# Kernel optimization log

Measured on AMD Instinct MI355X. Metric: run time of the kernel, lower is better.

## Reference

```python
import jax, jax.numpy as jnp
import numpy as np

EMBED_DIM = 512
NUM_HEADS = 8
GAMMA = 0.1


def setup_inputs() -> dict:
    key = jax.random.key(0)
    ks = jax.random.split(key, 16)
    B, T, D, Hp, Wp = 4, 16, EMBED_DIM, 24, 24
    Dq = D // 4
    s = 1.0 / np.sqrt(D)
    inp = {
        "h_opt": jax.random.normal(ks[0], (B, T, D, Hp, Wp), jnp.float32),
        "h_sar": jax.random.normal(ks[1], (B, T, D, Hp, Wp), jnp.float32),
        "Wq": jax.random.normal(ks[2], (D, D), jnp.float32) * s,
        "bq": jnp.zeros((D,), jnp.float32),
        "Wk": jax.random.normal(ks[3], (D, D), jnp.float32) * s,
        "bk": jnp.zeros((D,), jnp.float32),
        "Wv": jax.random.normal(ks[4], (D, D), jnp.float32) * s,
        "bv": jnp.zeros((D,), jnp.float32),
        "Wo": jax.random.normal(ks[5], (D, D), jnp.float32) * s,
        "bo": jnp.zeros((D,), jnp.float32),
        "Wp1": jax.random.normal(ks[6], (D, Dq), jnp.float32) * s,
        "bp1": jnp.zeros((Dq,), jnp.float32),
        "Wp2": jax.random.normal(ks[7], (Dq, 1), jnp.float32) * (1.0 / np.sqrt(Dq)),
        "bp2": jnp.zeros((1,), jnp.float32),
    }
    return inp


def reference(h_opt, h_sar, Wq, bq, Wk, bk, Wv, bv, Wo, bo, Wp1, bp1, Wp2, bp2):
    B, T, D, Hp, Wp_ = h_opt.shape
    S = Hp * Wp_
    H = NUM_HEADS
    hd = D // H

    # (B,T,D,H',W') -> (B*S, T, D): each spatial location is an independent sequence over T
    opt_seq = jnp.transpose(h_opt, (0, 3, 4, 1, 2)).reshape(B * S, T, D)
    sar_seq = jnp.transpose(h_sar, (0, 3, 4, 1, 2)).reshape(B * S, T, D)

    Q = (opt_seq @ Wq + bq).reshape(B * S, T, H, hd)
    K = (sar_seq @ Wk + bk).reshape(B * S, T, H, hd)
    V = (sar_seq @ Wv + bv).reshape(B * S, T, H, hd)

    # scores: (N, H, Tq, Tk)
    scores = jnp.einsum("nthd,nshd->nhts", Q, K) / np.sqrt(hd).astype(np.float32)

    # per-key physical violation penalty: MLP(sar) -> sigmoid in [0,1], shape (N, Tk)
    hdn = jax.nn.gelu(sar_seq @ Wp1 + bp1, approximate=False)
    p_viol = jax.nn.sigmoid((hdn @ Wp2 + bp2).squeeze(-1))  # (N, T)
    scores = scores - GAMMA * p_viol[:, None, None, :]

    attn = jax.nn.softmax(scores, axis=-1)  # dropout is identity in eval mode
    out = jnp.einsum("nhts,nshd->nthd", attn, V).reshape(B * S, T, D)
    out = out @ Wo + bo
    return jnp.transpose(out.reshape(B, Hp, Wp_, T, D), (0, 3, 4, 1, 2))
```

## Files before the change

### kernel.cpp

```cpp
#include <hip/hip_runtime.h>

#define GAMMA 0.1f

typedef unsigned short u16;
typedef u16 u16x8 __attribute__((ext_vector_type(8)));
typedef short s16x8 __attribute__((ext_vector_type(8)));
typedef float f32x4 __attribute__((ext_vector_type(4)));
typedef unsigned int ui32x4 __attribute__((ext_vector_type(4)));

__device__ __forceinline__ float b2f(u16 u) {
  return __uint_as_float(((unsigned)u) << 16);
}
__device__ __forceinline__ u16 f2bf(float f) {
  unsigned u = __float_as_uint(f);
  unsigned r = (u + 0x7FFFu + ((u >> 16) & 1u)) >> 16;
  return (u16)r;
}
__device__ __forceinline__ unsigned pk_bf16(float lo, float hi) {
  return (unsigned)f2bf(lo) | ((unsigned)f2bf(hi) << 16);
}

__device__ __forceinline__ void gl2lds16(const u16* g, u16* l) {
  __builtin_amdgcn_global_load_lds(
      (const __attribute__((address_space(1))) unsigned int*)g,
      (__attribute__((address_space(3))) unsigned int*)l, 16, 0, 0);
}

__device__ __forceinline__ int xcd_swz(int phys, int nwg) {
  return (phys & 7) * (nwg >> 3) + (phys >> 3);
}

__global__ __launch_bounds__(256) void transpose_k(
    const float* __restrict__ src, u16* __restrict__ dst, int K, int N)
{
  int idx = blockIdx.x * 256 + threadIdx.x;
  if (idx >= K * N) return;
  int nn = idx / K, kk = idx - nn * K;
  dst[idx] = f2bf(src[kk * N + nn]);
}

__global__ __launch_bounds__(256) void bias_kernel(
    const float* __restrict__ bq, const float* __restrict__ bk,
    const float* __restrict__ bv, const float* __restrict__ bp1,
    const float* __restrict__ bo,
    float* __restrict__ biasQ, float* __restrict__ biasKVP,
    float* __restrict__ biasO)
{
  int i = blockIdx.x * 256 + threadIdx.x;
  if (i < 512) {
    biasQ[i] = bq[i];
  } else if (i < 1664) {
    int j = i - 512;
    float v;
    if (j < 512) v = bk[j];
    else if (j < 1024) v = bv[j - 512];
    else v = bp1[j - 1024];
    biasKVP[j] = v;
  } else if (i < 2176) {
    biasO[i - 1664] = bo[i - 1664];
  }
}

__global__ __launch_bounds__(256) void convert_h(
    const float* __restrict__ h0, const float* __restrict__ h1,
    u16* __restrict__ d0, u16* __restrict__ d1)
{
  __shared__ __align__(16) u16 T[64 * 64];
  const int tid = threadIdx.x;
  const int kt = blockIdx.x & 7, st = blockIdx.x >> 3;
  const int bt = blockIdx.y;
  const float* src = (blockIdx.z ? h1 : h0) + (size_t)bt * (512 * 576);
  u16* dst = (blockIdx.z ? d1 : d0) + (size_t)bt * (576 * 512);

  const int s = tid & 63, kc = tid >> 6;
  const float* sp = src + (size_t)(kt * 64 + kc * 16) * 576 + st * 64 + s;
  unsigned pk[8];
#pragma unroll
  for (int i = 0; i < 8; ++i) {
    float lo = sp[(2 * i) * 576];
    float hi = sp[(2 * i + 1) * 576];
    pk[i] = pk_bf16(lo, hi);
  }
  ui32x4 v0 = {pk[0], pk[1], pk[2], pk[3]};
  ui32x4 v1 = {pk[4], pk[5], pk[6], pk[7]};
  *(ui32x4*)&T[s * 64 + (((kc * 2)     ^ (s & 7)) * 8)] = v0;
  *(ui32x4*)&T[s * 64 + (((kc * 2 + 1) ^ (s & 7)) * 8)] = v1;
  __syncthreads();
  const int r = tid >> 2, oc = (tid & 3) * 2;
  ui32x4 w0 = *(const ui32x4*)&T[r * 64 + ((oc       ^ (r & 7)) * 8)];
  ui32x4 w1 = *(const ui32x4*)&T[r * 64 + (((oc + 1) ^ (r & 7)) * 8)];
  u16* dp = dst + (size_t)(st * 64 + r) * 512 + kt * 64 + oc * 8;
  *(ui32x4*)dp = w0;
  *(ui32x4*)(dp + 8) = w1;
}

__global__ __launch_bounds__(256) void gemm_proj(
    const u16* __restrict__ hT, const u16* __restrict__ WT,
    const float* __restrict__ bias, u16* __restrict__ C, int NC)
{
  __shared__ __align__(16) u16 Al[2][64 * 64];
  __shared__ __align__(16) u16 Bl[2][128 * 64];
  const int tid = threadIdx.x;
  const int w = tid >> 6, lane = tid & 63;
  const int lhi = lane >> 4, llo = lane & 15;

  const int nwg = gridDim.x * gridDim.y;
  const int phys = blockIdx.y * gridDim.x + blockIdx.x;
  const int logical = xcd_swz(phys, nwg);
  const int bx = logical % gridDim.x;
  const int y = logical / gridDim.x;

  const int bt = y / 9, stile = y - bt * 9;
  const int s0 = stile * 64;
  const int col0 = bx * 128;

  const u16* Ab = hT + (size_t)bt * (576 * 512) + (size_t)s0 * 512;
  const u16* Bb = WT + (size_t)col0 * 512;

  const int brow = lane >> 3;
  const int bko = ((lane & 7) ^ brow) * 8;

  f32x4 acc[4][2];
#pragma unroll
  for (int mi = 0; mi < 4; ++mi)
#pragma unroll
    for (int ni = 0; ni < 2; ++ni)
#pragma unroll
      for (int e = 0; e < 4; ++e) acc[mi][ni][e] = 0.f;

#pragma unroll
  for (int i = 0; i < 2; ++i) {
    int q = w * 2 + i;
    gl2lds16(Ab + (size_t)(q * 8 + brow) * 512 + bko, &Al[0][q * 512]);
  }
#pragma unroll
  for (int i = 0; i < 4; ++i) {
    int q = w * 4 + i;
    gl2lds16(Bb + (size_t)(q * 8 + brow) * 512 + bko, &Bl[0][q * 512]);
  }

  for (int kt = 0; kt < 8; ++kt) {
    __syncthreads();
    if (kt < 7) {
      const int ktn = kt + 1;
#pragma unroll
      for (int i = 0; i < 2; ++i) {
        int q = w * 2 + i;
        gl2lds16(Ab + (size_t)(q * 8 + brow) * 512 + ktn * 64 + bko,
                 &Al[ktn & 1][q * 512]);
      }
#pragma unroll
      for (int i = 0; i < 4; ++i) {
        int q = w * 4 + i;
        gl2lds16(Bb + (size_t)(q * 8 + brow) * 512 + ktn * 64 + bko,
                 &Bl[ktn & 1][q * 512]);
      }
    }
    const u16* Alc = Al[kt & 1];
    const u16* Blc = Bl[kt & 1];
#pragma unroll
    for (int hh = 0; hh < 2; ++hh) {
      s16x8 af[4], bfr[2];
#pragma unroll
      for (int mi = 0; mi < 4; ++mi) {
        int row = mi * 16 + llo;
        af[mi] = *(const s16x8*)&Alc[row * 64 + ((((hh << 2) | lhi) ^ (row & 7)) * 8)];
      }
#pragma unroll
      for (int ni = 0; ni < 2; ++ni) {
        int n = w * 32 + ni * 16 + llo;
        bfr[ni] = *(const s16x8*)&Blc[n * 64 + ((((hh << 2) | lhi) ^ (n & 7)) * 8)];
      }
#pragma unroll
      for (int mi = 0; mi < 4; ++mi)
#pragma unroll
        for (int ni = 0; ni < 2; ++ni)
          acc[mi][ni] = __builtin_amdgcn_mfma_f32_16x16x32_bf16(
              af[mi], bfr[ni], acc[mi][ni], 0, 0, 0);
    }
  }

  const int b_ = bt >> 4, t_ = bt & 15;
  const size_t rowbase = (size_t)(b_ * 576 + s0) * 16 + t_;
  float bia0 = bias[col0 + w * 32 + llo];
  float bia1 = bias[col0 + w * 32 + 16 + llo];
#pragma unroll
  for (int mi = 0; mi < 4; ++mi) {
#pragma unroll
    for (int i = 0; i < 4; ++i) {
      const int m = mi * 16 + lhi * 4 + i;
      u16* cp = C + (rowbase + (size_t)m * 16) * NC + col0 + w * 32 + llo;
      cp[0]  = f2bf(acc[mi][0][i] + bia0);
      cp[16] = f2bf(acc[mi][1][i] + bia1);
    }
  }
}

__global__ __launch_bounds__(256) void pviol_kernel(
    const u16* __restrict__ KVP, const float* __restrict__ Wp2,
    const float* __restrict__ bp2, float* __restrict__ pv)
{
  const int tid = threadIdx.x;
  const int w = tid >> 6, lane = tid & 63;
  const int row = blockIdx.x * 4 + w;
  const int c = lane * 2;
  const u16* hp = KVP + (size_t)row * 1152 + 1024 + c;
  float x0 = b2f(hp[0]), x1 = b2f(hp[1]);
  float g0 = 0.5f * x0 * (1.f + erff(x0 * 0.70710678f));
  float g1 = 0.5f * x1 * (1.f + erff(x1 * 0.70710678f));
  float sum = g0 * Wp2[c] + g1 * Wp2[c + 1];
#pragma unroll
  for (int d = 1; d < 64; d <<= 1) sum += __shfl_xor(sum, d, 64);
  if (lane == 0) {
    float z = sum + bp2[0];
    pv[row] = 1.f / (1.f + expf(-z));
  }
}

__global__ __launch_bounds__(256) void attn_kernel(
    const u16* Q, const u16* __restrict__ KVP,
    const float* __restrict__ pviol, u16* att)
{
  __shared__ __align__(16) u16 Kl[4][16 * 72];
  __shared__ __align__(16) u16 Vl[4][16 * 72];
  __shared__ float Pl[4][16 * 17];
  const int tid = threadIdx.x;
  const int w = tid >> 6, lane = tid & 63;
  const int logical = xcd_swz(blockIdx.x, gridDim.x);
  const int wid = logical * 4 + w;
  const int n = wid >> 3, hh = wid & 7;
  const int g = lane >> 4, tq = lane & 15;

  const int r = lane >> 3, co = (lane & 7) * 8;
  const u16* Kb = KVP + (size_t)n * (16 * 1152) + hh * 64;
#pragma unroll
  for (int rr = 0; rr < 2; ++rr) {
    int row = r + rr * 8;
    *(u16x8*)&Kl[w][row * 72 + co] = *(const u16x8*)(Kb + row * 1152 + co);
    *(u16x8*)&Vl[w][row * 72 + co] = *(const u16x8*)(Kb + 512 + row * 1152 + co);
  }
  __syncthreads();

  float s[4] = {0.f, 0.f, 0.f, 0.f};
  const u16* Qr = Q + ((size_t)n * 16 + tq) * 512 + hh * 64;
  for (int kc = 0; kc < 8; ++kc) {
    u16x8 q8 = *(const u16x8*)(Qr + kc * 8);
    float qf[8];
#pragma unroll
    for (int j = 0; j < 8; ++j) qf[j] = b2f(q8[j]);
#pragma unroll
    for (int i = 0; i < 4; ++i) {
      u16x8 k8 = *(const u16x8*)&Kl[w][(g * 4 + i) * 72 + kc * 8];
#pragma unroll
      for (int j = 0; j < 8; ++j) s[i] += qf[j] * b2f(k8[j]);
    }
  }

  const float* pv = pviol + n * 16;
#pragma unroll
  for (int i = 0; i < 4; ++i) s[i] = s[i] * 0.125f - GAMMA * pv[g * 4 + i];

  float mx = fmaxf(fmaxf(s[0], s[1]), fmaxf(s[2], s[3]));
  mx = fmaxf(mx, __shfl_xor(mx, 16, 64));
  mx = fmaxf(mx, __shfl_xor(mx, 32, 64));
  float e[4], sum = 0.f;
#pragma unroll
  for (int i = 0; i < 4; ++i) { e[i] = expf(s[i] - mx); sum += e[i]; }
  sum += __shfl_xor(sum, 16, 64);
  sum += __shfl_xor(sum, 32, 64);
  float inv = 1.f / sum;
#pragma unroll
  for (int i = 0; i < 4; ++i) Pl[w][tq * 17 + g * 4 + i] = e[i] * inv;
  __syncthreads();

  float o[16];
#pragma unroll
  for (int j = 0; j < 16; ++j) o[j] = 0.f;
  for (int tk = 0; tk < 16; ++tk) {
    float p = Pl[w][tq * 17 + tk];
    u16x8 v0 = *(const u16x8*)&Vl[w][tk * 72 + g * 16];
    u16x8 v1 = *(const u16x8*)&Vl[w][tk * 72 + g * 16 + 8];
#pragma unroll
    for (int j = 0; j < 8; ++j) {
      o[j]     += p * b2f(v0[j]);
      o[8 + j] += p * b2f(v1[j]);
    }
  }
  u16* op = att + ((size_t)n * 16 + tq) * 512 + hh * 64 + g * 16;
  u16x8 r0, r1;
#pragma unroll
  for (int j = 0; j < 8; ++j) { r0[j] = f2bf(o[j]); r1[j] = f2bf(o[8 + j]); }
  *(u16x8*)op = r0;
  *(u16x8*)(op + 8) = r1;
}

__global__ __launch_bounds__(256) void gemm_out(
    const u16* __restrict__ A, const u16* __restrict__ WT,
    const float* __restrict__ bias, float* __restrict__ out)
{
  __shared__ __align__(16) char smem[49152];
  u16* Al0 = (u16*)smem;
  u16* Bl0 = (u16*)(smem + 16384);
  const int tid = threadIdx.x;
  const int w = tid >> 6, lane = tid & 63;
  const int lhi = lane >> 4, llo = lane & 15;

  const int nwg = gridDim.x * gridDim.y;
  const int phys = blockIdx.y * gridDim.x + blockIdx.x;
  const int logical = xcd_swz(phys, nwg);
  const int bx = logical % gridDim.x;
  const int y = logical / gridDim.x;

  const int bt = y / 9, stile = y - bt * 9;
  const int s0 = stile * 64;
  const int col0 = bx * 128;
  const int b_ = bt >> 4, t_ = bt & 15;

  const u16* Ab = A + ((size_t)(b_ * 576 + s0) * 16 + t_) * 512;
  const u16* Bb = WT + (size_t)col0 * 512;

  const int brow = lane >> 3;
  const int bko = ((lane & 7) ^ brow) * 8;

  f32x4 acc[4][2];
#pragma unroll
  for (int mi = 0; mi < 4; ++mi)
#pragma unroll
    for (int ni = 0; ni < 2; ++ni)
#pragma unroll
      for (int e = 0; e < 4; ++e) acc[mi][ni][e] = 0.f;

#pragma unroll
  for (int i = 0; i < 2; ++i) {
    int q = w * 2 + i;
    gl2lds16(Ab + (size_t)(q * 8 + brow) * (16 * 512) + bko, &Al0[q * 512]);
  }
#pragma unroll
  for (int i = 0; i < 4; ++i) {
    int q = w * 4 + i;
    gl2lds16(Bb + (size_t)(q * 8 + brow) * 512 + bko, &Bl0[q * 512]);
  }

  for (int kt = 0; kt < 8; ++kt) {
    __syncthreads();
    if (kt < 7) {
      const int ktn = kt + 1;
      u16* Ala = Al0 + (ktn & 1) * (64 * 64);
      u16* Bla = Bl0 + (ktn & 1) * (128 * 64);
#pragma unroll
      for (int i = 0; i < 2; ++i) {
        int q = w * 2 + i;
        gl2lds16(Ab + (size_t)(q * 8 + brow) * (16 * 512) + ktn * 64 + bko,
                 &Ala[q * 512]);
      }
#pragma unroll
      for (int i = 0; i < 4; ++i) {
        int q = w * 4 + i;
        gl2lds16(Bb + (size_t)(q * 8 + brow) * 512 + ktn * 64 + bko,
                 &Bla[q * 512]);
      }
    }
    const u16* Alc = Al0 + (kt & 1) * (64 * 64);
    const u16* Blc = Bl0 + (kt & 1) * (128 * 64);
#pragma unroll
    for (int hh = 0; hh < 2; ++hh) {
      s16x8 af[4], bfr[2];
#pragma unroll
      for (int mi = 0; mi < 4; ++mi) {
        int row = mi * 16 + llo;
        af[mi] = *(const s16x8*)&Alc[row * 64 + ((((hh << 2) | lhi) ^ (row & 7)) * 8)];
      }
#pragma unroll
      for (int ni = 0; ni < 2; ++ni) {
        int n = w * 32 + ni * 16 + llo;
        bfr[ni] = *(const s16x8*)&Blc[n * 64 + ((((hh << 2) | lhi) ^ (n & 7)) * 8)];
      }
#pragma unroll
      for (int mi = 0; mi < 4; ++mi)
#pragma unroll
        for (int ni = 0; ni < 2; ++ni)
          acc[mi][ni] = __builtin_amdgcn_mfma_f32_16x16x32_bf16(
              af[mi], bfr[ni], acc[mi][ni], 0, 0, 0);
    }
  }

  __syncthreads();
  float* Cl = (float*)smem;
  float bia0 = bias[col0 + w * 32 + llo];
  float bia1 = bias[col0 + w * 32 + 16 + llo];
#pragma unroll
  for (int mi = 0; mi < 4; ++mi)
#pragma unroll
    for (int i = 0; i < 4; ++i) {
      int m = mi * 16 + lhi * 4 + i;
      Cl[(w * 32 + llo) * 72 + m]      = acc[mi][0][i] + bia0;
      Cl[(w * 32 + 16 + llo) * 72 + m] = acc[mi][1][i] + bia1;
    }
  __syncthreads();
  const int nn = tid >> 1;
  const int mh = (tid & 1) * 32;
  const float* sp = Cl + nn * 72 + mh;
  float* dp = out + ((size_t)bt * 512 + col0 + nn) * 576 + s0 + mh;
#pragma unroll
  for (int j = 0; j < 8; ++j)
    *(float4*)(dp + j * 4) = *(const float4*)(sp + j * 4);
}

extern "C" void kernel_launch(void* const* d_in, const int* in_sizes, int n_in,
                              void* d_out, int out_size, void* d_ws, size_t ws_size,
                              hipStream_t stream)
{
  const float* h_opt = (const float*)d_in[0];
  const float* h_sar = (const float*)d_in[1];
  const float* Wq  = (const float*)d_in[2];
  const float* bq  = (const float*)d_in[3];
  const float* Wk  = (const float*)d_in[4];
  const float* bk  = (const float*)d_in[5];
  const float* Wv  = (const float*)d_in[6];
  const float* bv  = (const float*)d_in[7];
  const float* Wo  = (const float*)d_in[8];
  const float* bo  = (const float*)d_in[9];
  const float* Wp1 = (const float*)d_in[10];
  const float* bp1 = (const float*)d_in[11];
  const float* Wp2 = (const float*)d_in[12];
  const float* bp2 = (const float*)d_in[13];
  float* out = (float*)d_out;

  char* ws = (char*)d_ws;
  u16*   WqT     = (u16*)(ws + 0);
  u16*   KVPW    = (u16*)(ws + 524288);
  u16*   WoT     = (u16*)(ws + 1703936);
  float* biasQ   = (float*)(ws + 2228224);
  float* biasKVP = (float*)(ws + 2230272);
  float* biasO   = (float*)(ws + 2234880);
  float* pviol   = (float*)(ws + 2236928);
  u16*   Qbuf    = (u16*)(ws + 2384384);
  u16*   KVPbuf  = (u16*)(ws + 40133120);
  u16*   hTopt   = (u16*)(ws + 125067776);
  u16*   hTsar   = (u16*)(ws + 162816512);

  transpose_k<<<1024, 256, 0, stream>>>(Wq, WqT, 512, 512);
  transpose_k<<<1024, 256, 0, stream>>>(Wk, KVPW, 512, 512);
  transpose_k<<<1024, 256, 0, stream>>>(Wv, KVPW + 512 * 512, 512, 512);
  transpose_k<<<256, 256, 0, stream>>>(Wp1, KVPW + 1024 * 512, 512, 128);
  transpose_k<<<1024, 256, 0, stream>>>(Wo, WoT, 512, 512);
  bias_kernel<<<9, 256, 0, stream>>>(bq, bk, bv, bp1, bo, biasQ, biasKVP, biasO);
  convert_h<<<dim3(72, 64, 2), 256, 0, stream>>>(h_opt, h_sar, hTopt, hTsar);

  gemm_proj<<<dim3(4, 576), 256, 0, stream>>>(hTopt, WqT, biasQ, Qbuf, 512);
  gemm_proj<<<dim3(9, 576), 256, 0, stream>>>(hTsar, KVPW, biasKVP, KVPbuf, 1152);
  pviol_kernel<<<9216, 256, 0, stream>>>(KVPbuf, Wp2, bp2, pviol);
  attn_kernel<<<4608, 256, 0, stream>>>(Qbuf, KVPbuf, pviol, Qbuf);
  gemm_out<<<dim3(4, 576), 256, 0, stream>>>(Qbuf, WoT, biasO, out);
}
```

Before: 427.3 us.

## Merge prep kernels, fuse Q and KVP projections, fold p_viol MLP into GEMM epilogue

Seven prep launches (weight transposes, bias copies, h conversion) become one kernel that picks its role from the block index. The Q and K/V/P1 projection GEMMs are merged into a single 13-column grid. The GELU+Wp2+sigmoid violation head is computed in the epilogue of the P1 column tile, which removes the separate pviol kernel and the bf16 write and reread of the P1 hidden activations. This cuts launch overhead and memory traffic, and keeps the hidden activations in fp32 instead of rounding them to bf16. The cost is extra branching, extra shared memory and shuffle reductions in the GEMM kernel.

```diff
diff --git a/kernel.cpp b/kernel.cpp
--- a/kernel.cpp
+++ b/kernel.cpp
@@ -30,92 +30,130 @@
   return (phys & 7) * (nwg >> 3) + (phys >> 3);
 }
 
-__global__ __launch_bounds__(256) void transpose_k(
-    const float* __restrict__ src, u16* __restrict__ dst, int K, int N)
+#define PREP_NCONV 9216
+#define PREP_T0 9216
+#define PREP_T1 10240
+#define PREP_T2 11264
+#define PREP_T3 12288
+#define PREP_T4 12544
+#define PREP_T5 13568
+#define PREP_NB 13577
+
+__device__ __forceinline__ void tr_block(
+    const float* __restrict__ src, u16* __restrict__ dst, int N, int blk, int tid)
 {
-  int idx = blockIdx.x * 256 + threadIdx.x;
-  if (idx >= K * N) return;
-  int nn = idx / K, kk = idx - nn * K;
+  int idx = blk * 256 + tid;
+  int nn = idx >> 9, kk = idx & 511;
   dst[idx] = f2bf(src[kk * N + nn]);
 }
 
-__global__ __launch_bounds__(256) void bias_kernel(
+__global__ __launch_bounds__(256) void prep_all(
+    const float* __restrict__ h0, const float* __restrict__ h1,
+    u16* __restrict__ d0, u16* __restrict__ d1,
+    const float* __restrict__ Wq, const float* __restrict__ Wk,
+    const float* __restrict__ Wv, const float* __restrict__ Wp1,
+    const float* __restrict__ Wo,
     const float* __restrict__ bq, const float* __restrict__ bk,
     const float* __restrict__ bv, const float* __restrict__ bp1,
     const float* __restrict__ bo,
+    u16* __restrict__ WqT, u16* __restrict__ KVPW, u16* __restrict__ WoT,
     float* __restrict__ biasQ, float* __restrict__ biasKVP,
     float* __restrict__ biasO)
 {
-  int i = blockIdx.x * 256 + threadIdx.x;
-  if (i < 512) {
-    biasQ[i] = bq[i];
-  } else if (i < 1664) {
-    int j = i - 512;
-    float v;
-    if (j < 512) v = bk[j];
-    else if (j < 1024) v = bv[j - 512];
-    else v = bp1[j - 1024];
-    biasKVP[j] = v;
-  } else if (i < 2176) {
-    biasO[i - 1664] = bo[i - 1664];
-  }
-}
-
-__global__ __launch_bounds__(256) void convert_h(
-    const float* __restrict__ h0, const float* __restrict__ h1,
-    u16* __restrict__ d0, u16* __restrict__ d1)
-{
   __shared__ __align__(16) u16 T[64 * 64];
+  const int b = blockIdx.x;
   const int tid = threadIdx.x;
-  const int kt = blockIdx.x & 7, st = blockIdx.x >> 3;
-  const int bt = blockIdx.y;
-  const float* src = (blockIdx.z ? h1 : h0) + (size_t)bt * (512 * 576);
-  u16* dst = (blockIdx.z ? d1 : d0) + (size_t)bt * (576 * 512);
-
-  const int s = tid & 63, kc = tid >> 6;
-  const float* sp = src + (size_t)(kt * 64 + kc * 16) * 576 + st * 64 + s;
-  unsigned pk[8];
-#pragma unroll
-  for (int i = 0; i < 8; ++i) {
-    float lo = sp[(2 * i) * 576];
-    float hi = sp[(2 * i + 1) * 576];
-    pk[i] = pk_bf16(lo, hi);
-  }
-  ui32x4 v0 = {pk[0], pk[1], pk[2], pk[3]};
-  ui32x4 v1 = {pk[4], pk[5], pk[6], pk[7]};
-  *(ui32x4*)&T[s * 64 + (((kc * 2)     ^ (s & 7)) * 8)] = v0;
-  *(ui32x4*)&T[s * 64 + (((kc * 2 + 1) ^ (s & 7)) * 8)] = v1;
-  __syncthreads();
-  const int r = tid >> 2, oc = (tid & 3) * 2;
-  ui32x4 w0 = *(const ui32x4*)&T[r * 64 + ((oc       ^ (r & 7)) * 8)];
-  ui32x4 w1 = *(const ui32x4*)&T[r * 64 + (((oc + 1) ^ (r & 7)) * 8)];
-  u16* dp = dst + (size_t)(st * 64 + r) * 512 + kt * 64 + oc * 8;
-  *(ui32x4*)dp = w0;
-  *(ui32x4*)(dp + 8) = w1;
-}
-
-__global__ __launch_bounds__(256) void gemm_proj(
-    const u16* __restrict__ hT, const u16* __restrict__ WT,
-    const float* __restrict__ bias, u16* __restrict__ C, int NC)
+
+  if (b < PREP_NCONV) {
+    const int z = b / 4608;
+    const int r_ = b - z * 4608;
+    const int bt = r_ / 72;
+    const int xx = r_ - bt * 72;
+    const int kt = xx & 7, st = xx >> 3;
+    const float* src = (z ? h1 : h0) + (size_t)bt * (512 * 576);
+    u16* dst = (z ? d1 : d0) + (size_t)bt * (576 * 512);
+
+    const int s = tid & 63, kc = tid >> 6;
+    const float* sp = src + (size_t)(kt * 64 + kc * 16) * 576 + st * 64 + s;
+    unsigned pk[8];
+#pragma unroll
+    for (int i = 0; i < 8; ++i) {
+      float lo = sp[(2 * i) * 576];
+      float hi = sp[(2 * i + 1) * 576];
+      pk[i] = pk_bf16(lo, hi);
+    }
+    ui32x4 v0 = {pk[0], pk[1], pk[2], pk[3]};
+    ui32x4 v1 = {pk[4], pk[5], pk[6], pk[7]};
+    *(ui32x4*)&T[s * 64 + (((kc * 2)     ^ (s & 7)) * 8)] = v0;
+    *(ui32x4*)&T[s * 64 + (((kc * 2 + 1) ^ (s & 7)) * 8)] = v1;
+    __syncthreads();
+    const int r = tid >> 2, oc = (tid & 3) * 2;
+    ui32x4 w0 = *(const ui32x4*)&T[r * 64 + ((oc       ^ (r & 7)) * 8)];
+    ui32x4 w1 = *(const ui32x4*)&T[r * 64 + (((oc + 1) ^ (r & 7)) * 8)];
+    u16* dp = dst + (size_t)(st * 64 + r) * 512 + kt * 64 + oc * 8;
+    *(ui32x4*)dp = w0;
+    *(ui32x4*)(dp + 8) = w1;
+  } else if (b < PREP_T1) {
+    tr_block(Wq, WqT, 512, b - PREP_T0, tid);
+  } else if (b < PREP_T2) {
+    tr_block(Wk, KVPW, 512, b - PREP_T1, tid);
+  } else if (b < PREP_T3) {
+    tr_block(Wv, KVPW + 512 * 512, 512, b - PREP_T2, tid);
+  } else if (b < PREP_T4) {
+    tr_block(Wp1, KVPW + 1024 * 512, 128, b - PREP_T3, tid);
+  } else if (b < PREP_T5) {
+    tr_block(Wo, WoT, 512, b - PREP_T4, tid);
+  } else {
+    int i = (b - PREP_T5) * 256 + tid;
+    if (i < 512) {
+      biasQ[i] = bq[i];
+    } else if (i < 1664) {
+      int j = i - 512;
+      float v;
+      if (j < 512) v = bk[j];
+      else if (j < 1024) v = bv[j - 512];
+      else v = bp1[j - 1024];
+      biasKVP[j] = v;
+    } else if (i < 2176) {
+      biasO[i - 1664] = bo[i - 1664];
+    }
+  }
+}
+
+__global__ __launch_bounds__(256) void gemm_proj_all(
+    const u16* __restrict__ hTopt, const u16* __restrict__ hTsar,
+    const u16* __restrict__ WqT, const u16* __restrict__ KVPW,
+    const float* __restrict__ biasQ, const float* __restrict__ biasKVP,
+    const float* __restrict__ Wp2, const float* __restrict__ bp2,
+    u16* __restrict__ Qbuf, u16* __restrict__ KVPbuf,
+    float* __restrict__ pviol)
 {
   __shared__ __align__(16) u16 Al[2][64 * 64];
   __shared__ __align__(16) u16 Bl[2][128 * 64];
+  __shared__ float Pv[256];
   const int tid = threadIdx.x;
   const int w = tid >> 6, lane = tid & 63;
   const int lhi = lane >> 4, llo = lane & 15;
 
-  const int nwg = gridDim.x * gridDim.y;
-  const int phys = blockIdx.y * gridDim.x + blockIdx.x;
+  const int nwg = 13 * 576;
+  const int phys = blockIdx.y * 13 + blockIdx.x;
   const int logical = xcd_swz(phys, nwg);
-  const int bx = logical % gridDim.x;
-  const int y = logical / gridDim.x;
+  const int bx = logical % 13;
+  const int y = logical / 13;
 
   const int bt = y / 9, stile = y - bt * 9;
   const int s0 = stile * 64;
-  const int col0 = bx * 128;
-
-  const u16* Ab = hT + (size_t)bt * (576 * 512) + (size_t)s0 * 512;
-  const u16* Bb = WT + (size_t)col0 * 512;
+
+  const bool isQ = (bx < 4);
+  const int bxl = isQ ? bx : bx - 4;
+  const int col0 = bxl * 128;
+  const int NC = isQ ? 512 : 1152;
+  const u16* Ab = (isQ ? hTopt : hTsar) + (size_t)bt * (576 * 512)
+                  + (size_t)s0 * 512;
+  const u16* Bb = (isQ ? WqT : KVPW) + (size_t)col0 * 512;
+  const float* bias = isQ ? biasQ : biasKVP;
+  u16* C = isQ ? Qbuf : KVPbuf;
+  const bool dopv = (!isQ) && (bxl == 8);
 
   const int brow = lane >> 3;
   const int bko = ((lane & 7) ^ brow) * 8;
@@ -184,36 +222,50 @@
   const size_t rowbase = (size_t)(b_ * 576 + s0) * 16 + t_;
   float bia0 = bias[col0 + w * 32 + llo];
   float bia1 = bias[col0 + w * 32 + 16 + llo];
-#pragma unroll
-  for (int mi = 0; mi < 4; ++mi) {
-#pragma unroll
-    for (int i = 0; i < 4; ++i) {
-      const int m = mi * 16 + lhi * 4 + i;
-      u16* cp = C + (rowbase + (size_t)m * 16) * NC + col0 + w * 32 + llo;
-      cp[0]  = f2bf(acc[mi][0][i] + bia0);
-      cp[16] = f2bf(acc[mi][1][i] + bia1);
-    }
-  }
-}
-
-__global__ __launch_bounds__(256) void pviol_kernel(
-    const u16* __restrict__ KVP, const float* __restrict__ Wp2,
-    const float* __restrict__ bp2, float* __restrict__ pv)
-{
-  const int tid = threadIdx.x;
-  const int w = tid >> 6, lane = tid & 63;
-  const int row = blockIdx.x * 4 + w;
-  const int c = lane * 2;
-  const u16* hp = KVP + (size_t)row * 1152 + 1024 + c;
-  float x0 = b2f(hp[0]), x1 = b2f(hp[1]);
-  float g0 = 0.5f * x0 * (1.f + erff(x0 * 0.70710678f));
-  float g1 = 0.5f * x1 * (1.f + erff(x1 * 0.70710678f));
-  float sum = g0 * Wp2[c] + g1 * Wp2[c + 1];
-#pragma unroll
-  for (int d = 1; d < 64; d <<= 1) sum += __shfl_xor(sum, d, 64);
-  if (lane == 0) {
-    float z = sum + bp2[0];
-    pv[row] = 1.f / (1.f + expf(-z));
+
+  if (dopv) {
+    const float w2a = Wp2[w * 32 + llo];
+    const float w2b = Wp2[w * 32 + 16 + llo];
+    float part[16];
+#pragma unroll
+    for (int mi = 0; mi < 4; ++mi)
+#pragma unroll
+      for (int i = 0; i < 4; ++i) {
+        float x0 = acc[mi][0][i] + bia0;
+        float x1 = acc[mi][1][i] + bia1;
+        float g0 = 0.5f * x0 * (1.f + erff(x0 * 0.70710678f));
+        float g1 = 0.5f * x1 * (1.f + erff(x1 * 0.70710678f));
+        part[mi * 4 + i] = g0 * w2a + g1 * w2b;
+      }
+#pragma unroll
+    for (int d = 1; d < 16; d <<= 1)
+#pragma unroll
+      for (int idx = 0; idx < 16; ++idx)
+        part[idx] += __shfl_xor(part[idx], d, 64);
+    if (llo == 0) {
+#pragma unroll
+      for (int mi = 0; mi < 4; ++mi)
+#pragma unroll
+        for (int i = 0; i < 4; ++i)
+          Pv[w * 64 + mi * 16 + lhi * 4 + i] = part[mi * 4 + i];
+    }
+    __syncthreads();
+    if (tid < 64) {
+      float sum = Pv[tid] + Pv[64 + tid] + Pv[128 + tid] + Pv[192 + tid]
+                  + bp2[0];
+      pviol[rowbase + (size_t)tid * 16] = 1.f / (1.f + expf(-sum));
+    }
+  } else {
+#pragma unroll
+    for (int mi = 0; mi < 4; ++mi) {
+#pragma unroll
+      for (int i = 0; i < 4; ++i) {
+        const int m = mi * 16 + lhi * 4 + i;
+        u16* cp = C + (rowbase + (size_t)m * 16) * NC + col0 + w * 32 + llo;
+        cp[0]  = f2bf(acc[mi][0][i] + bia0);
+        cp[16] = f2bf(acc[mi][1][i] + bia1);
+      }
+    }
   }
 }
 
@@ -439,17 +491,14 @@
   u16*   hTopt   = (u16*)(ws + 125067776);
   u16*   hTsar   = (u16*)(ws + 162816512);
 
-  transpose_k<<<1024, 256, 0, stream>>>(Wq, WqT, 512, 512);
-  transpose_k<<<1024, 256, 0, stream>>>(Wk, KVPW, 512, 512);
-  transpose_k<<<1024, 256, 0, stream>>>(Wv, KVPW + 512 * 512, 512, 512);
-  transpose_k<<<256, 256, 0, stream>>>(Wp1, KVPW + 1024 * 512, 512, 128);
-  transpose_k<<<1024, 256, 0, stream>>>(Wo, WoT, 512, 512);
-  bias_kernel<<<9, 256, 0, stream>>>(bq, bk, bv, bp1, bo, biasQ, biasKVP, biasO);
-  convert_h<<<dim3(72, 64, 2), 256, 0, stream>>>(h_opt, h_sar, hTopt, hTsar);
-
-  gemm_proj<<<dim3(4, 576), 256, 0, stream>>>(hTopt, WqT, biasQ, Qbuf, 512);
-  gemm_proj<<<dim3(9, 576), 256, 0, stream>>>(hTsar, KVPW, biasKVP, KVPbuf, 1152);
-  pviol_kernel<<<9216, 256, 0, stream>>>(KVPbuf, Wp2, bp2, pviol);
+  prep_all<<<PREP_NB, 256, 0, stream>>>(
+      h_opt, h_sar, hTopt, hTsar, Wq, Wk, Wv, Wp1, Wo,
+      bq, bk, bv, bp1, bo, WqT, KVPW, WoT, biasQ, biasKVP, biasO);
+
+  gemm_proj_all<<<dim3(13, 576), 256, 0, stream>>>(
+      hTopt, hTsar, WqT, KVPW, biasQ, biasKVP, Wp2, bp2,
+      Qbuf, KVPbuf, pviol);
+
   attn_kernel<<<4608, 256, 0, stream>>>(Qbuf, KVPbuf, pviol, Qbuf);
   gemm_out<<<dim3(4, 576), 256, 0, stream>>>(Qbuf, WoT, biasO, out);
 }
```

Result: faster. 408.0 us (-4.5%).
